# Kernel optimization log

Hardware: AMD Instinct MI355X
Metric: run time of the kernel (lower is better)

The kernel has to match this reference:

```python
import jax, jax.numpy as jnp
import numpy as np

N_NODES = 50000
N_EDGES = 800000
D = 128


def _gcn_layer(x, src, dst, deg_inv_sqrt, W, b, n_nodes):
    # GCNConv: X' = D^{-1/2} (A + I) D^{-1/2} X W + b   (PyG default, self-loops added)
    h = x @ W  # [N, D]
    norm = deg_inv_sqrt[src] * deg_inv_sqrt[dst]  # [E+N]
    msgs = h[src] * norm[:, None]  # [E+N, D] gather + scale
    out = jax.ops.segment_sum(msgs, dst, num_segments=n_nodes)  # scatter-add
    return out + b


def setup_inputs() -> dict:
    key = jax.random.key(0)
    k1, k2, k3, k4 = jax.random.split(key, 4)
    x = jax.random.normal(k1, (N_NODES, D), dtype=jnp.float32)
    edge_index = jax.random.randint(k2, (2, N_EDGES), 0, N_NODES, dtype=jnp.int64)
    scale = 1.0 / np.sqrt(D)
    W1 = jax.random.normal(k3, (D, D), dtype=jnp.float32) * scale
    b1 = jnp.zeros((D,), dtype=jnp.float32)
    W2 = jax.random.normal(k4, (D, D), dtype=jnp.float32) * scale
    b2 = jnp.zeros((D,), dtype=jnp.float32)
    return {"x": x, "edge_index": edge_index, "W1": W1, "b1": b1, "W2": W2, "b2": b2}


def reference(x, edge_index, W1, b1, W2, b2):
    n_nodes = x.shape[0]
    # add self-loops once (same graph both layers)
    loop = jnp.arange(n_nodes, dtype=edge_index.dtype)
    src = jnp.concatenate([edge_index[0], loop])
    dst = jnp.concatenate([edge_index[1], loop])
    deg = jax.ops.segment_sum(jnp.ones_like(dst, dtype=x.dtype), dst, num_segments=n_nodes)
    deg_inv_sqrt = jnp.where(deg > 0, jax.lax.rsqrt(deg), 0.0)

    h = _gcn_layer(x, src, dst, deg_inv_sqrt, W1, b1, n_nodes)
    h = jax.nn.relu(h)
    h = _gcn_layer(h, src, dst, deg_inv_sqrt, W2, b2, n_nodes)
    h = jax.nn.relu(h)
    return h
```

## Files before the change

### kernel.cpp

```cpp
#include <hip/hip_runtime.h>

#define N_NODES 50000
#define N_EDGES 800000
#define D 128
#define NB 196
#define CHUNK 4096
#define NBKT 196
#define LHM (NBKT * NB)
#define NSB 151

typedef unsigned int uint32;
typedef unsigned short ushort;
typedef __attribute__((ext_vector_type(8))) short s8v;
typedef __attribute__((ext_vector_type(4))) float f4v;

__device__ __forceinline__ ushort f2bf(float f) {
    unsigned u = __float_as_uint(f);
    u += 0x7FFFu + ((u >> 16) & 1u);
    return (ushort)(u >> 16);
}
__device__ __forceinline__ float bf_lo(uint32 u) { return __uint_as_float(u << 16); }
__device__ __forceinline__ float bf_hi(uint32 u) { return __uint_as_float(u & 0xFFFF0000u); }

__device__ __forceinline__ int block_incl_scan(int v, int t) {
    int lane = t & 63, wv = t >> 6;
    int incl = v;
    #pragma unroll
    for (int off = 1; off < 64; off <<= 1) {
        int u = __shfl_up(incl, off, 64);
        if (lane >= off) incl += u;
    }
    __shared__ int wsums[4];
    if (lane == 63) wsums[wv] = incl;
    __syncthreads();
    int add = 0;
    if (wv > 0) add += wsums[0];
    if (wv > 1) add += wsums[1];
    if (wv > 2) add += wsums[2];
    return incl + add;
}

__global__ __launch_bounds__(256) void phaseA_kernel(const int* __restrict__ dst,
                                                     int* __restrict__ histM) {
    __shared__ int cnt[NBKT];
    int t = threadIdx.x, blk = blockIdx.x;
    if (t < NBKT) cnt[t] = 0;
    __syncthreads();
    int e0 = blk * CHUNK;
    for (int i = t; i < CHUNK; i += 256) {
        int e = e0 + i;
        if (e < N_EDGES) atomicAdd(&cnt[dst[e] >> 8], 1);
    }
    __syncthreads();
    if (t < NBKT) histM[t * NB + blk] = cnt[t];
}

__global__ __launch_bounds__(256) void scan1g(const int* __restrict__ in,
                                              int* __restrict__ out,
                                              int* __restrict__ bsum) {
    int t = threadIdx.x, blk = blockIdx.x;
    int i = blk * 256 + t;
    int v = (i < LHM) ? in[i] : 0;
    int incl = block_incl_scan(v, t);
    if (i < LHM) out[i] = incl - v;
    if (t == 255) bsum[blk] = incl;
}
__global__ __launch_bounds__(256) void scan2g(const int* __restrict__ bsum,
                                              int* __restrict__ boff) {
    int t = threadIdx.x;
    int v = (t < NSB) ? bsum[t] : 0;
    int incl = block_incl_scan(v, t);
    if (t < NSB) boff[t] = incl - v;
}
__global__ __launch_bounds__(256) void scan3g(int* __restrict__ out,
                                              const int* __restrict__ boff) {
    int i = blockIdx.x * 256 + threadIdx.x;
    if (i < LHM) out[i] += boff[blockIdx.x];
}

__global__ __launch_bounds__(256) void phaseC_kernel(const int* __restrict__ src,
                                                     const int* __restrict__ dst,
                                                     const int* __restrict__ base,
                                                     uint32* __restrict__ edgeTmp) {
    __shared__ int cur[NBKT];
    int t = threadIdx.x, blk = blockIdx.x;
    if (t < NBKT) cur[t] = base[t * NB + blk];
    __syncthreads();
    int e0 = blk * CHUNK;
    for (int i = t; i < CHUNK; i += 256) {
        int e = e0 + i;
        if (e < N_EDGES) {
            uint32 s = (uint32)src[e], d = (uint32)dst[e];
            int p = atomicAdd(&cur[d >> 8], 1);
            edgeTmp[p] = (s << 16) | d;
        }
    }
}

__global__ __launch_bounds__(256) void phaseD_kernel(const uint32* __restrict__ edgeTmp,
                                                     const int* __restrict__ base,
                                                     int* __restrict__ rowstart,
                                                     float* __restrict__ dis,
                                                     ushort* __restrict__ e16) {
    __shared__ int cnt[256];
    __shared__ int cur[256];
    int t = threadIdx.x, b = blockIdx.x;
    int beg = base[b * NB];
    int end = (b == NBKT - 1) ? N_EDGES : base[(b + 1) * NB];
    cnt[t] = 0;
    __syncthreads();
    for (int p = beg + t; p < end; p += 256)
        atomicAdd(&cnt[edgeTmp[p] & 255], 1);
    __syncthreads();
    int c = cnt[t];
    int incl = block_incl_scan(c, t);
    int excl = incl - c;
    int node = b * 256 + t;
    if (node <= N_NODES) rowstart[node] = beg + excl;
    if (node < N_NODES) dis[node] = rsqrtf((float)(c + 1));
    cur[t] = excl;
    __syncthreads();
    for (int p = beg + t; p < end; p += 256) {
        uint32 u = edgeTmp[p];
        int r = atomicAdd(&cur[u & 255], 1);
        e16[beg + r] = (ushort)(u >> 16);
    }
}

__global__ __launch_bounds__(256) void wprep_kernel(const float* __restrict__ W1,
                                                    const float* __restrict__ W2,
                                                    ushort* __restrict__ W1t,
                                                    ushort* __restrict__ W2t) {
    const float* W = blockIdx.x ? W2 : W1;
    ushort* Wt = blockIdx.x ? W2t : W1t;
    int t = threadIdx.x;
    #pragma unroll
    for (int it = 0; it < 16; it++) {
        int fid = t + it * 256;
        int k = fid >> 5;
        int n0 = (fid & 31) * 4;
        float4 w = ((const float4*)W)[fid];
        Wt[(n0 + 0) * D + k] = f2bf(w.x);
        Wt[(n0 + 1) * D + k] = f2bf(w.y);
        Wt[(n0 + 2) * D + k] = f2bf(w.z);
        Wt[(n0 + 3) * D + k] = f2bf(w.w);
    }
}

__global__ __launch_bounds__(256) void gemm_mfma(const float* __restrict__ X,
                                                 const ushort* __restrict__ Wt,
                                                 const float* __restrict__ dis,
                                                 ushort* __restrict__ Hb) {
    __shared__ ushort Cs[128 * 136];
    int t = threadIdx.x;
    int wv = t >> 6, lane = t & 63;
    int q = lane >> 4, m = lane & 15;
    int rbase = blockIdx.x * 128 + wv * 32;
    f4v zero = {0.f, 0.f, 0.f, 0.f};
    f4v acc[2][8];
    #pragma unroll
    for (int mt = 0; mt < 2; mt++)
        #pragma unroll
        for (int n = 0; n < 8; n++) acc[mt][n] = zero;

    #pragma unroll
    for (int kt = 0; kt < 4; kt++) {
        int k0 = kt * 32 + q * 8;
        s8v a[2];
        #pragma unroll
        for (int mt = 0; mt < 2; mt++) {
            int row = rbase + mt * 16 + m;
            if (row >= N_NODES) row = N_NODES - 1;
            const float* xp = X + (size_t)row * D + k0;
            float4 u0 = *(const float4*)xp;
            float4 u1 = *(const float4*)(xp + 4);
            s8v av;
            av[0] = (short)f2bf(u0.x); av[1] = (short)f2bf(u0.y);
            av[2] = (short)f2bf(u0.z); av[3] = (short)f2bf(u0.w);
            av[4] = (short)f2bf(u1.x); av[5] = (short)f2bf(u1.y);
            av[6] = (short)f2bf(u1.z); av[7] = (short)f2bf(u1.w);
            a[mt] = av;
        }
        #pragma unroll
        for (int n = 0; n < 8; n++) {
            s8v b = *(const s8v*)(Wt + (size_t)(n * 16 + m) * D + k0);
            acc[0][n] = __builtin_amdgcn_mfma_f32_16x16x32_bf16(a[0], b, acc[0][n], 0, 0, 0);
            acc[1][n] = __builtin_amdgcn_mfma_f32_16x16x32_bf16(a[1], b, acc[1][n], 0, 0, 0);
        }
    }
    float disv[2][4];
    #pragma unroll
    for (int mt = 0; mt < 2; mt++)
        #pragma unroll
        for (int r = 0; r < 4; r++) {
            int row = rbase + mt * 16 + q * 4 + r;
            if (row >= N_NODES) row = N_NODES - 1;
            disv[mt][r] = dis[row];
        }
    #pragma unroll
    for (int mt = 0; mt < 2; mt++)
        #pragma unroll
        for (int n = 0; n < 8; n++)
            #pragma unroll
            for (int r = 0; r < 4; r++) {
                int row = wv * 32 + mt * 16 + q * 4 + r;
                Cs[row * 136 + n * 16 + m] = f2bf(acc[mt][n][r] * disv[mt][r]);
            }
    __syncthreads();
    int gbase = blockIdx.x * 128;
    #pragma unroll
    for (int it = 0; it < 8; it++) {
        int cid = t + it * 256;
        int row = cid >> 4, off = (cid & 15) * 8;
        int grow = gbase + row;
        if (grow < N_NODES) {
            s8v v = *(const s8v*)(Cs + row * 136 + off);
            *(s8v*)(Hb + (size_t)grow * D + off) = v;
        }
    }
}

__global__ __launch_bounds__(256) void aggr_kernel(const uint32* __restrict__ Hb,
                                                   const float* __restrict__ dis,
                                                   const int* __restrict__ rowstart,
                                                   const ushort* __restrict__ e16,
                                                   const float* __restrict__ bias,
                                                   float* __restrict__ Hout) {
    int n = blockIdx.x * 4 + (threadIdx.x >> 6);
    if (n >= N_NODES) return;
    int t = threadIdx.x & 63;
    float dn = dis[n];
    uint32 us = Hb[(size_t)n * 64 + t];
    float ax = bf_lo(us), ay = bf_hi(us);
    int beg = rowstart[n], end = rowstart[n + 1];
    int p = beg;
    for (; p + 7 < end; p += 8) {
        int s0 = e16[p + 0], s1 = e16[p + 1], s2 = e16[p + 2], s3 = e16[p + 3];
        int s4 = e16[p + 4], s5 = e16[p + 5], s6 = e16[p + 6], s7 = e16[p + 7];
        uint32 u0 = Hb[(size_t)s0 * 64 + t];
        uint32 u1 = Hb[(size_t)s1 * 64 + t];
        uint32 u2 = Hb[(size_t)s2 * 64 + t];
        uint32 u3 = Hb[(size_t)s3 * 64 + t];
        uint32 u4 = Hb[(size_t)s4 * 64 + t];
        uint32 u5 = Hb[(size_t)s5 * 64 + t];
        uint32 u6 = Hb[(size_t)s6 * 64 + t];
        uint32 u7 = Hb[(size_t)s7 * 64 + t];
        ax += bf_lo(u0) + bf_lo(u1) + bf_lo(u2) + bf_lo(u3)
            + bf_lo(u4) + bf_lo(u5) + bf_lo(u6) + bf_lo(u7);
        ay += bf_hi(u0) + bf_hi(u1) + bf_hi(u2) + bf_hi(u3)
            + bf_hi(u4) + bf_hi(u5) + bf_hi(u6) + bf_hi(u7);
    }
    for (; p < end; p++) {
        uint32 u0 = Hb[(size_t)e16[p] * 64 + t];
        ax += bf_lo(u0); ay += bf_hi(u0);
    }
    float2 bb = ((const float2*)bias)[t];
    float2 o;
    o.x = fmaxf(fmaf(dn, ax, bb.x), 0.f);
    o.y = fmaxf(fmaf(dn, ay, bb.y), 0.f);
    ((float2*)Hout)[(size_t)n * 64 + t] = o;
}

extern "C" void kernel_launch(void* const* d_in, const int* in_sizes, int n_in,
                              void* d_out, int out_size, void* d_ws, size_t ws_size,
                              hipStream_t stream) {
    const float* x  = (const float*)d_in[0];
    const int*   ei = (const int*)d_in[1];
    const float* W1 = (const float*)d_in[2];
    const float* b1 = (const float*)d_in[3];
    const float* W2 = (const float*)d_in[4];
    const float* b2 = (const float*)d_in[5];
    float* out = (float*)d_out;

    char* ws = (char*)d_ws;
    size_t off = 0;
    auto alloc = [&](size_t bytes) -> void* {
        void* p = ws + off;
        off += (bytes + 255) & ~(size_t)255;
        return p;
    };
    int*    histM    = (int*)alloc((size_t)LHM * 4);
    int*    base     = (int*)alloc((size_t)LHM * 4);
    int*    bsum     = (int*)alloc(256 * 4);
    int*    boff     = (int*)alloc(256 * 4);
    int*    rowstart = (int*)alloc((size_t)(N_NODES + 1) * 4);
    float*  dis      = (float*)alloc((size_t)N_NODES * 4);
    uint32* edgeTmp  = (uint32*)alloc((size_t)N_EDGES * 4);
    ushort* e16      = (ushort*)alloc((size_t)N_EDGES * 2);
    ushort* Hb       = (ushort*)alloc((size_t)N_NODES * D * 2);
    float*  HO1      = (float*)alloc((size_t)N_NODES * D * 4);
    ushort* W1t      = (ushort*)alloc((size_t)D * D * 2);
    ushort* W2t      = (ushort*)alloc((size_t)D * D * 2);

    const int* src = ei;
    const int* dst = ei + N_EDGES;

    wprep_kernel<<<2, 256, 0, stream>>>(W1, W2, W1t, W2t);
    phaseA_kernel<<<NB, 256, 0, stream>>>(dst, histM);
    scan1g<<<NSB, 256, 0, stream>>>(histM, base, bsum);
    scan2g<<<1, 256, 0, stream>>>(bsum, boff);
    scan3g<<<NSB, 256, 0, stream>>>(base, boff);
    phaseC_kernel<<<NB, 256, 0, stream>>>(src, dst, base, edgeTmp);
    phaseD_kernel<<<NBKT, 256, 0, stream>>>(edgeTmp, base, rowstart, dis, e16);

    gemm_mfma<<<(N_NODES + 127) / 128, 256, 0, stream>>>(x, W1t, dis, Hb);
    aggr_kernel<<<(N_NODES + 3) / 4, 256, 0, stream>>>((const uint32*)Hb, dis, rowstart,
                                                       e16, b1, HO1);
    gemm_mfma<<<(N_NODES + 127) / 128, 256, 0, stream>>>(HO1, W2t, dis, Hb);
    aggr_kernel<<<(N_NODES + 3) / 4, 256, 0, stream>>>((const uint32*)Hb, dis, rowstart,
                                                       e16, b2, out);
}
```

Baseline: 235.0 us.

## Store layer-1 output in bf16 and widen aggregation gathers to 16-byte loads

The intermediate activation between the two layers is now written as bf16 by the first aggregation, and the second GEMM reads it directly without converting from fp32. That halves the intermediate's write and read traffic. The aggregation kernel is restructured so 16 lanes per node each load a uint4 (8 bf16 values) instead of 64 lanes each loading 32 bits, which puts 16 nodes in each block. The extra bf16 rounding of the intermediate adds a small precision loss, and the inner edge unroll drops from 8 to 4.

```diff
diff --git a/kernel.cpp b/kernel.cpp
--- a/kernel.cpp
+++ b/kernel.cpp
@@ -147,7 +147,8 @@
     }
 }
 
-__global__ __launch_bounds__(256) void gemm_mfma(const float* __restrict__ X,
+template<bool BF16IN>
+__global__ __launch_bounds__(256) void gemm_mfma(const void* __restrict__ Xv,
                                                  const ushort* __restrict__ Wt,
                                                  const float* __restrict__ dis,
                                                  ushort* __restrict__ Hb) {
@@ -171,15 +172,20 @@
         for (int mt = 0; mt < 2; mt++) {
             int row = rbase + mt * 16 + m;
             if (row >= N_NODES) row = N_NODES - 1;
-            const float* xp = X + (size_t)row * D + k0;
-            float4 u0 = *(const float4*)xp;
-            float4 u1 = *(const float4*)(xp + 4);
-            s8v av;
-            av[0] = (short)f2bf(u0.x); av[1] = (short)f2bf(u0.y);
-            av[2] = (short)f2bf(u0.z); av[3] = (short)f2bf(u0.w);
-            av[4] = (short)f2bf(u1.x); av[5] = (short)f2bf(u1.y);
-            av[6] = (short)f2bf(u1.z); av[7] = (short)f2bf(u1.w);
-            a[mt] = av;
+            if (BF16IN) {
+                const ushort* xp = (const ushort*)Xv + (size_t)row * D + k0;
+                a[mt] = *(const s8v*)xp;
+            } else {
+                const float* xp = (const float*)Xv + (size_t)row * D + k0;
+                float4 u0 = *(const float4*)xp;
+                float4 u1 = *(const float4*)(xp + 4);
+                s8v av;
+                av[0] = (short)f2bf(u0.x); av[1] = (short)f2bf(u0.y);
+                av[2] = (short)f2bf(u0.z); av[3] = (short)f2bf(u0.w);
+                av[4] = (short)f2bf(u1.x); av[5] = (short)f2bf(u1.y);
+                av[6] = (short)f2bf(u1.z); av[7] = (short)f2bf(u1.w);
+                a[mt] = av;
+            }
         }
         #pragma unroll
         for (int n = 0; n < 8; n++) {
@@ -220,45 +226,70 @@
     }
 }
 
-__global__ __launch_bounds__(256) void aggr_kernel(const uint32* __restrict__ Hb,
+__device__ __forceinline__ void acc8(float* a, uint4 v) {
+    a[0] += bf_lo(v.x); a[1] += bf_hi(v.x);
+    a[2] += bf_lo(v.y); a[3] += bf_hi(v.y);
+    a[4] += bf_lo(v.z); a[5] += bf_hi(v.z);
+    a[6] += bf_lo(v.w); a[7] += bf_hi(v.w);
+}
+
+template<bool BF16OUT>
+__global__ __launch_bounds__(256) void aggr_kernel(const uint4* __restrict__ Hb4,
                                                    const float* __restrict__ dis,
                                                    const int* __restrict__ rowstart,
                                                    const ushort* __restrict__ e16,
                                                    const float* __restrict__ bias,
-                                                   float* __restrict__ Hout) {
-    int n = blockIdx.x * 4 + (threadIdx.x >> 6);
-    if (n >= N_NODES) return;
-    int t = threadIdx.x & 63;
+                                                   void* __restrict__ Hout) {
+    int t = threadIdx.x;
+    int li = t & 15;
+    int n = blockIdx.x * 16 + (t >> 4);
     float dn = dis[n];
-    uint32 us = Hb[(size_t)n * 64 + t];
-    float ax = bf_lo(us), ay = bf_hi(us);
+    float a[8];
+    {
+        uint4 sv = Hb4[(size_t)n * 16 + li];
+        a[0] = bf_lo(sv.x); a[1] = bf_hi(sv.x);
+        a[2] = bf_lo(sv.y); a[3] = bf_hi(sv.y);
+        a[4] = bf_lo(sv.z); a[5] = bf_hi(sv.z);
+        a[6] = bf_lo(sv.w); a[7] = bf_hi(sv.w);
+    }
     int beg = rowstart[n], end = rowstart[n + 1];
     int p = beg;
-    for (; p + 7 < end; p += 8) {
+    for (; p + 3 < end; p += 4) {
         int s0 = e16[p + 0], s1 = e16[p + 1], s2 = e16[p + 2], s3 = e16[p + 3];
-        int s4 = e16[p + 4], s5 = e16[p + 5], s6 = e16[p + 6], s7 = e16[p + 7];
-        uint32 u0 = Hb[(size_t)s0 * 64 + t];
-        uint32 u1 = Hb[(size_t)s1 * 64 + t];
-        uint32 u2 = Hb[(size_t)s2 * 64 + t];
-        uint32 u3 = Hb[(size_t)s3 * 64 + t];
-        uint32 u4 = Hb[(size_t)s4 * 64 + t];
-        uint32 u5 = Hb[(size_t)s5 * 64 + t];
-        uint32 u6 = Hb[(size_t)s6 * 64 + t];
-        uint32 u7 = Hb[(size_t)s7 * 64 + t];
-        ax += bf_lo(u0) + bf_lo(u1) + bf_lo(u2) + bf_lo(u3)
-            + bf_lo(u4) + bf_lo(u5) + bf_lo(u6) + bf_lo(u7);
-        ay += bf_hi(u0) + bf_hi(u1) + bf_hi(u2) + bf_hi(u3)
-            + bf_hi(u4) + bf_hi(u5) + bf_hi(u6) + bf_hi(u7);
+        uint4 v0 = Hb4[(size_t)s0 * 16 + li];
+        uint4 v1 = Hb4[(size_t)s1 * 16 + li];
+        uint4 v2 = Hb4[(size_t)s2 * 16 + li];
+        uint4 v3 = Hb4[(size_t)s3 * 16 + li];
+        acc8(a, v0); acc8(a, v1); acc8(a, v2); acc8(a, v3);
     }
     for (; p < end; p++) {
-        uint32 u0 = Hb[(size_t)e16[p] * 64 + t];
-        ax += bf_lo(u0); ay += bf_hi(u0);
-    }
-    float2 bb = ((const float2*)bias)[t];
-    float2 o;
-    o.x = fmaxf(fmaf(dn, ax, bb.x), 0.f);
-    o.y = fmaxf(fmaf(dn, ay, bb.y), 0.f);
-    ((float2*)Hout)[(size_t)n * 64 + t] = o;
+        uint4 v0 = Hb4[(size_t)e16[p] * 16 + li];
+        acc8(a, v0);
+    }
+    const float4* b4 = (const float4*)bias;
+    float4 bb0 = b4[li * 2], bb1 = b4[li * 2 + 1];
+    float r0 = fmaxf(fmaf(dn, a[0], bb0.x), 0.f);
+    float r1 = fmaxf(fmaf(dn, a[1], bb0.y), 0.f);
+    float r2 = fmaxf(fmaf(dn, a[2], bb0.z), 0.f);
+    float r3 = fmaxf(fmaf(dn, a[3], bb0.w), 0.f);
+    float r4 = fmaxf(fmaf(dn, a[4], bb1.x), 0.f);
+    float r5 = fmaxf(fmaf(dn, a[5], bb1.y), 0.f);
+    float r6 = fmaxf(fmaf(dn, a[6], bb1.z), 0.f);
+    float r7 = fmaxf(fmaf(dn, a[7], bb1.w), 0.f);
+    if (BF16OUT) {
+        uint4 o;
+        o.x = (uint32)f2bf(r0) | ((uint32)f2bf(r1) << 16);
+        o.y = (uint32)f2bf(r2) | ((uint32)f2bf(r3) << 16);
+        o.z = (uint32)f2bf(r4) | ((uint32)f2bf(r5) << 16);
+        o.w = (uint32)f2bf(r6) | ((uint32)f2bf(r7) << 16);
+        ((uint4*)Hout)[(size_t)n * 16 + li] = o;
+    } else {
+        float4* H4 = (float4*)Hout;
+        float4 o0; o0.x = r0; o0.y = r1; o0.z = r2; o0.w = r3;
+        float4 o1; o1.x = r4; o1.y = r5; o1.z = r6; o1.w = r7;
+        H4[(size_t)n * 32 + li * 2]     = o0;
+        H4[(size_t)n * 32 + li * 2 + 1] = o1;
+    }
 }
 
 extern "C" void kernel_launch(void* const* d_in, const int* in_sizes, int n_in,
@@ -288,7 +319,7 @@
     uint32* edgeTmp  = (uint32*)alloc((size_t)N_EDGES * 4);
     ushort* e16      = (ushort*)alloc((size_t)N_EDGES * 2);
     ushort* Hb       = (ushort*)alloc((size_t)N_NODES * D * 2);
-    float*  HO1      = (float*)alloc((size_t)N_NODES * D * 4);
+    ushort* HO1      = (ushort*)alloc((size_t)N_NODES * D * 2);
     ushort* W1t      = (ushort*)alloc((size_t)D * D * 2);
     ushort* W2t      = (ushort*)alloc((size_t)D * D * 2);
 
@@ -303,10 +334,10 @@
     phaseC_kernel<<<NB, 256, 0, stream>>>(src, dst, base, edgeTmp);
     phaseD_kernel<<<NBKT, 256, 0, stream>>>(edgeTmp, base, rowstart, dis, e16);
 
-    gemm_mfma<<<(N_NODES + 127) / 128, 256, 0, stream>>>(x, W1t, dis, Hb);
-    aggr_kernel<<<(N_NODES + 3) / 4, 256, 0, stream>>>((const uint32*)Hb, dis, rowstart,
-                                                       e16, b1, HO1);
-    gemm_mfma<<<(N_NODES + 127) / 128, 256, 0, stream>>>(HO1, W2t, dis, Hb);
-    aggr_kernel<<<(N_NODES + 3) / 4, 256, 0, stream>>>((const uint32*)Hb, dis, rowstart,
-                                                       e16, b2, out);
-}
+    gemm_mfma<false><<<(N_NODES + 127) / 128, 256, 0, stream>>>(x, W1t, dis, Hb);
+    aggr_kernel<true><<<N_NODES / 16, 256, 0, stream>>>((const uint4*)Hb, dis, rowstart,
+                                                        e16, b1, HO1);
+    gemm_mfma<true><<<(N_NODES + 127) / 128, 256, 0, stream>>>(HO1, W2t, dis, Hb);
+    aggr_kernel<false><<<N_NODES / 16, 256, 0, stream>>>((const uint4*)Hb, dis, rowstart,
+                                                         e16, b2, out);
+}
```

New measurement: 216.4 us. 7.9% less time.
